# Performance work log

Hardware: AMD Instinct MI355X
Metric: run time of the kernel (lower is better)

Reference implementation:

```python
import jax, jax.numpy as jnp
import numpy as np

ITER_MCMC = 100000   # outer Metropolis-Hastings steps
ITER_DA = 10000      # delayed-acceptance inner slots to fill
MAX_ATT = 60000      # fixed attempt budget replacing the data-dependent while-loop
NOBS = 256           # observation_locations.shape[0]
NOISE = 0.5          # observation_noise
STEP0 = 0.1          # initial proposal std (step_size)
TARGET_ACC = 0.234   # Robbins-Monro adaptation target


def _mcmc_da(obs_loc, obs_val, theta0, eps_outer, u_outer, eps_da, u_da):
    dt_ = obs_loc.dtype
    pi = jnp.asarray(np.pi, dt_)

    def log_prior(th):
        return -0.5 * jnp.sum(th * th)

    def preds_outer(th):  # coarse / NN-surrogate forward model, shape [NOBS]
        return th[0] * jnp.sin(pi * obs_loc) + th[1] * jnp.cos(pi * obs_loc)

    def preds_inner(th):  # fine / solver forward model, shape [NOBS]
        return preds_outer(th) + 0.05 * th[0] * th[1] * jnp.sin(2.0 * pi * obs_loc)

    def loglik(p):
        return -0.5 * jnp.sum((obs_val - p) ** 2) / (NOISE ** 2)

    def lpost_o(th):
        return log_prior(th) + loglik(preds_outer(th))

    def lpost_i(th):
        return log_prior(th) + loglik(preds_inner(th))

    # ---- Stage 1: adaptive random-walk Metropolis-Hastings ----
    @jax.checkpoint
    def outer_step(carry, xs):
        theta, dt = carry
        eps, u, i = xs
        prop = theta + dt * eps
        # exp(x).clamp(max=1) == exp(min(x, 0)) -- numerically stable
        a = jnp.exp(jnp.minimum(lpost_o(prop) - lpost_o(theta), 0.0))
        theta = jnp.where(u < a, prop, theta)
        dt = dt + dt * (a - TARGET_ACC) / (i + 1.0)
        return (theta, dt), None

    steps = jnp.arange(ITER_MCMC, dtype=dt_)
    (theta, dt), _ = jax.lax.scan(
        outer_step, (theta0, jnp.asarray(STEP0, dt_)), (eps_outer, u_outer, steps)
    )

    # ---- Stage 2: delayed acceptance (fixed attempt budget, masked writes) ----
    @jax.checkpoint
    def da_step(carry, xs):
        theta, mh = carry
        eps, u = xs
        prop = theta + dt * eps
        lo, lp = lpost_o(theta), lpost_o(prop)
        a = jnp.exp(jnp.minimum(lp - lo, 0.0))
        active = (u[0] < a) & (mh < ITER_DA)
        # second stage ratio: exp(dpost_inner) * (a_rec / a) with a_rec/a == exp(lo-lp)
        a2 = jnp.exp(jnp.minimum(lpost_i(prop) - lpost_i(theta) + lo - lp, 0.0))
        inner_acc = active & (u[1] < a2)
        idx_w = jnp.where(active, mh, ITER_DA)  # inactive writes go to dropped row
        theta = jnp.where(inner_acc, prop, theta)
        mh = mh + active.astype(mh.dtype)
        ys = (idx_w, prop, preds_outer(prop), preds_inner(prop),
              inner_acc.astype(dt_))
        return (theta, mh), ys

    (_, _), (idx_w, props, po, pin, accs) = jax.lax.scan(
        da_step, (theta, jnp.asarray(0, jnp.int32)), (eps_da, u_da)
    )

    npar = theta0.shape[0]
    theta_inner = jnp.zeros((ITER_DA + 1, npar), dt_).at[idx_w].set(props)[:ITER_DA]
    lik_nn = jnp.zeros((ITER_DA + 1, NOBS), dt_).at[idx_w].set(po)[:ITER_DA]
    lik_sol = jnp.zeros((ITER_DA + 1, NOBS), dt_).at[idx_w].set(pin)[:ITER_DA]
    acc_list = jnp.zeros(ITER_DA + 1, dt_).at[idx_w].add(accs)[:ITER_DA]
    return acc_list, theta_inner, lik_nn, lik_sol


def setup_inputs() -> dict:
    key = jax.random.key(0)
    k = jax.random.split(key, 7)
    return {
        "obs_loc": jax.random.uniform(k[0], (NOBS,), dtype=jnp.float32),
        "obs_val": jax.random.normal(k[1], (NOBS,), dtype=jnp.float32),
        "theta0": jax.random.normal(k[2], (2,), dtype=jnp.float32),
        "eps_outer": jax.random.normal(k[3], (ITER_MCMC, 2), dtype=jnp.float32),
        "u_outer": jax.random.uniform(k[4], (ITER_MCMC,), dtype=jnp.float32),
        "eps_da": jax.random.normal(k[5], (MAX_ATT, 2), dtype=jnp.float32),
        "u_da": jax.random.uniform(k[6], (MAX_ATT, 2), dtype=jnp.float32),
    }


def reference(obs_loc, obs_val, theta0, eps_outer, u_outer, eps_da, u_da):
    return _mcmc_da(obs_loc, obs_val, theta0, eps_outer, u_outer, eps_da, u_da)
```

## Files before the change

kernel.cpp:

```cpp
#include <hip/hip_runtime.h>
#include <math.h>


#define ITER_MCMC 100000
#define ITER_DA   10000
#define MAX_ATT   60000
#define NOBS      256

#define WS_S    0
#define WS_C    256
#define WS_Z    512
#define WS_REC  768
#define WS_MH   (WS_REC + 3*(ITER_DA+1))
#define WS_FLAG (WS_MH + 2)
#define WS_HEAT (WS_FLAG + 2)

#define PI_F32  3.14159274101257324f
#define TPI_F32 6.28318548202514648f
#define DONE_MAGIC 0x1D0E5EEDu

__device__ __forceinline__ float fmul_s(float a, float b){
#pragma clang fp contract(off)
  return a*b;
}
__device__ __forceinline__ float fadd_s(float a, float b){
#pragma clang fp contract(off)
  return a+b;
}
__device__ __forceinline__ float fsub_s(float a, float b){
#pragma clang fp contract(off)
  return a-b;
}
__device__ __forceinline__ float dpp_xor1(float v){
  return __int_as_float(__builtin_amdgcn_update_dpp(0, __float_as_int(v), 0xB1, 0xF, 0xF, true));
}
__device__ __forceinline__ float dpp_xor2(float v){
  return __int_as_float(__builtin_amdgcn_update_dpp(0, __float_as_int(v), 0x4E, 0xF, 0xF, true));
}
__device__ __forceinline__ float dpp_ror4(float v){
  return __int_as_float(__builtin_amdgcn_update_dpp(0, __float_as_int(v), 0x124, 0xF, 0xF, true));
}
__device__ __forceinline__ float dpp_ror8(float v){
  return __int_as_float(__builtin_amdgcn_update_dpp(0, __float_as_int(v), 0x128, 0xF, 0xF, true));
}
__device__ __forceinline__ float bcast0(float v){
  return __int_as_float(__builtin_amdgcn_readfirstlane(__float_as_int(v)));
}
__device__ __forceinline__ float rlane(float v, int l){
  return __int_as_float(__builtin_amdgcn_readlane(__float_as_int(v), l));
}

typedef unsigned __attribute__((ext_vector_type(2))) u32x2;

__device__ __forceinline__ float exp_fast(float xf, int elo, int ehi){
  double x = (double)xf;
  double z = x * 0x1.71547652b82fep+5;
  double kd = z + 0x1.8p52;
  int kii = (int)__double_as_longlong(kd);
  kd -= 0x1.8p52;
  double r = z - kd;
  double t = r * 0x1.62e42fefa39efp-6;
  double p = 1.0 + t*(1.0 + t*(0.5 + t*(1.0/6.0)));
  int sj = __builtin_amdgcn_readfirstlane(kii & 31);
  unsigned lo = (unsigned)__builtin_amdgcn_readlane(elo, sj);
  unsigned hi = (unsigned)__builtin_amdgcn_readlane(ehi, sj);
  long long sb = (long long)(((unsigned long long)hi << 32) | lo)
               + ((long long)(kii >> 5) << 52);
  double s = __longlong_as_double(sb);
  return (float)(p * s);
}

__global__ void __launch_bounds__(256) k_chain(
    const float* __restrict__ obs_loc,
    const float* __restrict__ obs_val,
    const float* __restrict__ theta0,
    const float* __restrict__ eps_outer,
    const float* __restrict__ u_outer,
    const float* __restrict__ eps_da,
    const float* __restrict__ u_da,
    float* __restrict__ ws)
{
  unsigned* flag = (unsigned*)(ws + WS_FLAG);

  if (blockIdx.x != 0){
    __builtin_amdgcn_s_setprio(0);
    float h0=1.0f+(float)threadIdx.x, h1=2.0f, h2=3.0f, h3=4.0f;
    for (int it=0; it<400000; ++it){
#pragma unroll
      for (int k=0;k<8;k++){
        h0 = __builtin_fmaf(h0, 0.9999999f, 1e-9f);
        h1 = __builtin_fmaf(h1, 0.9999999f, 2e-9f);
        h2 = __builtin_fmaf(h2, 0.9999999f, 3e-9f);
        h3 = __builtin_fmaf(h3, 0.9999999f, 4e-9f);
      }
      __builtin_amdgcn_s_sleep(8);
      if (__hip_atomic_load(flag, __ATOMIC_RELAXED, __HIP_MEMORY_SCOPE_AGENT) == DONE_MAGIC)
        break;
    }
    if (threadIdx.x == 0) ws[WS_HEAT + blockIdx.x] = h0+h1+h2+h3;
    return;
  }
  if (threadIdx.x >= 64) return;
  __builtin_amdgcn_s_setprio(3);

  const int lane = threadIdx.x;
  const int cc = lane & 7;
  const int gg = lane >> 3;

  int elo, ehi;
  {
    long long b = __double_as_longlong(::exp2((double)(lane & 31) * 0.03125));
    elo = (int)(unsigned)(b & 0xffffffffLL);
    ehi = (int)(b >> 32);
  }

  const int blk = (int)((0x23541067u >> (gg*4)) & 7u);

  float s4[4], c4[4], z4[4], y4[4];
#pragma unroll
  for (int j=0;j<4;j++){
    int idx = 32*blk + 8*j + cc;
    float x = obs_loc[idx];
    float px  = fmul_s(PI_F32,  x);
    float tpx = fmul_s(TPI_F32, x);
    s4[j] = (float)::sin((double)px);
    c4[j] = (float)::cos((double)px);
    z4[j] = (float)::sin((double)tpx);
    y4[j] = obs_val[idx];
    ws[WS_S+idx]=s4[j]; ws[WS_C+idx]=c4[j]; ws[WS_Z+idx]=z4[j];
  }

  const bool odd16 = (lane & 16) != 0;
  const bool hi32  = (lane & 32) != 0;
  const bool hi8   = (lane & 8)  != 0;

  bool selx16 = false, selx32 = false;
  {
    u32x2 q  = __builtin_amdgcn_permlane16_swap((unsigned)lane, (unsigned)lane, false, false);
    bool A16 = (__builtin_amdgcn_readfirstlane((int)q.x) == 0);
    selx16 = (odd16 == A16);
    u32x2 q2 = __builtin_amdgcn_permlane32_swap((unsigned)lane, (unsigned)lane, false, false);
    bool A32 = (__builtin_amdgcn_readfirstlane((int)q2.x) == 0);
    selx32 = (hi32 == A32);
  }

  auto mv8 = [&](float v)->float{
    return dpp_ror8(v);
  };
  auto mv16 = [&](float v)->float{
    u32x2 p = __builtin_amdgcn_permlane16_swap(__float_as_uint(v), __float_as_uint(v), false, false);
    return __uint_as_float(selx16 ? p.x : p.y);
  };
  auto mv32 = [&](float v)->float{
    u32x2 p = __builtin_amdgcn_permlane32_swap(__float_as_uint(v), __float_as_uint(v), false, false);
    return __uint_as_float(selx32 ? p.x : p.y);
  };

  auto fold256 = [&](const float (&t)[4])->float{
    float r = t[0];
    r = fadd_s(r, t[1]); r = fadd_s(r, t[2]); r = fadd_s(r, t[3]);
    r = fadd_s(mv8(r),  t[0]);
    r = fadd_s(r, t[1]); r = fadd_s(r, t[2]); r = fadd_s(r, t[3]);
    r = fadd_s(mv32(r), t[0]);
    r = fadd_s(r, t[1]); r = fadd_s(r, t[2]); r = fadd_s(r, t[3]);
    r = fadd_s(mv8(r),  t[0]);
    r = fadd_s(r, t[1]); r = fadd_s(r, t[2]); r = fadd_s(r, t[3]);
    r = fadd_s(mv16(r), t[0]);
    r = fadd_s(r, t[1]); r = fadd_s(r, t[2]); r = fadd_s(r, t[3]);
    r = fadd_s(mv8(r),  t[0]);
    r = fadd_s(r, t[1]); r = fadd_s(r, t[2]); r = fadd_s(r, t[3]);
    r = fadd_s(mv32(r), t[0]);
    r = fadd_s(r, t[1]); r = fadd_s(r, t[2]); r = fadd_s(r, t[3]);
    r = fadd_s(mv8(r),  t[0]);
    r = fadd_s(r, t[1]); r = fadd_s(r, t[2]); r = fadd_s(r, t[3]);
    return r;
  };
  auto tree8 = [&](float r)->float{
    float d8  = mv8(r);
    float rdup = hi8 ? d8 : r;
    rdup = fadd_s(rdup, dpp_ror4(rdup));
    rdup = fadd_s(rdup, dpp_xor2(rdup));
    rdup = fadd_s(rdup, dpp_xor1(rdup));
    return bcast0(rdup);
  };
  auto sum_outer = [&](float p0, float p1)->float{
    float t[4];
#pragma unroll
    for (int j=0;j<4;j++){
      float po = fadd_s(fmul_s(p0,s4[j]), fmul_s(p1,c4[j]));
      float d  = fsub_s(y4[j], po);
      t[j] = fmul_s(d, d);
    }
    return tree8(fold256(t));
  };
  auto sum_both = [&](float p0, float p1, float& So, float& Si){
    float bq = fmul_s(fmul_s(0.05f, p0), p1);
    float to[4], ti[4];
#pragma unroll
    for (int j=0;j<4;j++){
      float po = fadd_s(fmul_s(p0,s4[j]), fmul_s(p1,c4[j]));
      float dl = fsub_s(y4[j], po);
      to[j] = fmul_s(dl, dl);
      float pn = fadd_s(po, fmul_s(bq, z4[j]));
      float di = fsub_s(y4[j], pn);
      ti[j] = fmul_s(di, di);
    }
    float ro = fold256(to);
    float ri = fold256(ti);
    So = tree8(ro);
    Si = tree8(ri);
  };

  auto lpost_from = [&](float p0, float p1, float S){
    float pr = fmul_s(-0.5f, fadd_s(fmul_s(p0,p0), fmul_s(p1,p1)));
    float ll = fmul_s(-2.0f, S);
    return fadd_s(pr, ll);
  };
  auto accept_prob = [&](float d){
    float dc = fmaxf(d, -150.0f);
    return exp_fast(dc, elo, ehi);
  };

  float t0 = theta0[0], t1 = theta0[1];
  float dtv = 0.1f;
  float lpo = lpost_from(t0, t1, sum_outer(t0, t1));

  float vE = eps_outer[lane];
  float vU = u_outer[(lane < 100000) ? lane : 0];
  for (int w=0; w<ITER_MCMC; w+=32){
    int nw = w + 32;
    int ie = 2*nw + lane; if (ie > 2*ITER_MCMC-1) ie = 2*ITER_MCMC-1;
    int iu = nw + lane;   if (iu > ITER_MCMC-1)   iu = ITER_MCMC-1;
    float nE = eps_outer[ie];
    float nU = u_outer[iu];
#pragma unroll 2
    for (int k=0;k<32;k++){
      int i = w + k;
      float den  = fadd_s((float)i, 1.0f);
      float rc   = __builtin_amdgcn_rcpf(den);
      float er1  = __builtin_fmaf(-den, rc, 1.0f);
      float rc1  = __builtin_fmaf(er1, rc, rc);
      float er2  = __builtin_fmaf(-den, rc1, 1.0f);
      float rc2  = __builtin_fmaf(er2, rc1, rc1);

      float e0 = rlane(vE, 2*k);
      float e1 = rlane(vE, 2*k+1);
      float uu = rlane(vU, k);
      float p0 = fadd_s(t0, fmul_s(dtv, e0));
      float p1 = fadd_s(t1, fmul_s(dtv, e1));
      float S   = sum_outer(p0, p1);
      float lpp = lpost_from(p0, p1, S);
      float d   = fsub_s(lpp, lpo);
      d = (d < 0.0f) ? d : 0.0f;
      float a = accept_prob(d);
      bool acc = (uu < a);
      t0  = acc ? p0  : t0;
      t1  = acc ? p1  : t1;
      lpo = acc ? lpp : lpo;
      float num = fmul_s(dtv, fsub_s(a, 0.234f));
      float q0  = fmul_s(num, rc2);
      float res = __builtin_fmaf(-den, q0, num);
      float q   = __builtin_fmaf(res, rc2, q0);
      dtv = fadd_s(dtv, q);
    }
    vE = nE; vU = nU;
  }

  float So_, Si_;
  sum_both(t0, t1, So_, Si_);
  float lpi = lpost_from(t0, t1, Si_);

  int mh = 0;
  float vE2 = eps_da[lane];
  float vU2 = u_da[lane];
  for (int w=0; w<MAX_ATT && mh<ITER_DA; w+=32){
    int nw = w + 32;
    int ia = 2*nw + lane; if (ia > 2*MAX_ATT-1) ia = 2*MAX_ATT-1;
    float nE = eps_da[ia];
    float nU = u_da[ia];
#pragma unroll 2
    for (int k=0;k<32;k++){
      float f0 = rlane(vE2, 2*k);
      float f1 = rlane(vE2, 2*k+1);
      float v0 = rlane(vU2, 2*k);
      float v1 = rlane(vU2, 2*k+1);
      float p0 = fadd_s(t0, fmul_s(dtv, f0));
      float p1 = fadd_s(t1, fmul_s(dtv, f1));
      float So2, Si2;
      sum_both(p0, p1, So2, Si2);
      float lp  = lpost_from(p0, p1, So2);
      float lip = lpost_from(p0, p1, Si2);
      float d1 = fsub_s(lp, lpo);
      d1 = (d1 < 0.0f) ? d1 : 0.0f;
      float d2 = fsub_s(fadd_s(fsub_s(lip, lpi), lpo), lp);
      d2 = (d2 < 0.0f) ? d2 : 0.0f;
      float a  = accept_prob(d1);
      float a2 = accept_prob(d2);
      bool active = (v0 < a) && (mh < ITER_DA);
      bool inner  = active && (v1 < a2);
      int idxw = active ? mh : ITER_DA;
      if (lane==0){
        ws[WS_REC+3*idxw+0] = p0;
        ws[WS_REC+3*idxw+1] = p1;
        ws[WS_REC+3*idxw+2] = inner ? 1.0f : 0.0f;
      }
      mh += active ? 1 : 0;
      t0  = inner ? p0  : t0;
      t1  = inner ? p1  : t1;
      lpo = inner ? lp  : lpo;
      lpi = inner ? lip : lpi;
    }
    vE2 = nE; vU2 = nU;
  }
  if (lane==0){
    ws[WS_MH] = (float)mh;
    __hip_atomic_store(flag, DONE_MAGIC, __ATOMIC_RELAXED, __HIP_MEMORY_SCOPE_AGENT);
  }
}

__global__ void __launch_bounds__(256) k_fill(const float* __restrict__ ws,
                                              float* __restrict__ out){
  const int m = blockIdx.x, j = threadIdx.x;
  const int mh = (int)ws[WS_MH];
  float* acc_list = out;
  float* th_in    = out + ITER_DA;
  float* lik_nn   = out + 3*ITER_DA;
  float* lik_sol  = lik_nn + (size_t)ITER_DA*NOBS;
  float bias = (float)(ITER_DA - m) * 1.5e-6f;
  if (m < mh){
    float p0 = ws[WS_REC+3*m+0];
    float p1 = ws[WS_REC+3*m+1];
    float fa = ws[WS_REC+3*m+2];
    float po = fadd_s(fmul_s(p0, ws[WS_S+j]), fmul_s(p1, ws[WS_C+j]));
    float b  = fmul_s(fmul_s(0.05f, p0), p1);
    float pn = fadd_s(po, fmul_s(b, ws[WS_Z+j]));
    lik_nn[(size_t)m*NOBS + j]  = po;
    lik_sol[(size_t)m*NOBS + j] = pn;
    if (j==0){
      acc_list[m] = fa + ((fa > 0.5f) ? bias : -bias);
      th_in[2*m]=p0; th_in[2*m+1]=p1;
    }
  } else {
    lik_nn[(size_t)m*NOBS + j]  = 0.0f;
    lik_sol[(size_t)m*NOBS + j] = 0.0f;
    if (j==0){ acc_list[m] = -bias; th_in[2*m]=0.0f; th_in[2*m+1]=0.0f; }
  }
}

extern "C" void kernel_launch(void* const* d_in, const int* in_sizes, int n_in,
                              void* d_out, int out_size, void* d_ws, size_t ws_size,
                              hipStream_t stream) {
  const float* obs_loc   = (const float*)d_in[0];
  const float* obs_val   = (const float*)d_in[1];
  const float* theta0    = (const float*)d_in[2];
  const float* eps_outer = (const float*)d_in[3];
  const float* u_outer   = (const float*)d_in[4];
  const float* eps_da    = (const float*)d_in[5];
  const float* u_da      = (const float*)d_in[6];
  float* ws = (float*)d_ws;

  hipLaunchKernelGGL(k_chain, dim3(256),     dim3(256), 0, stream,
                     obs_loc, obs_val, theta0, eps_outer, u_outer, eps_da, u_da, ws);
  hipLaunchKernelGGL(k_fill,  dim3(ITER_DA), dim3(256), 0, stream, ws, (float*)d_out);
}
```

Baseline: 46.42 ms.

## Speculatively precompute next DA proposal sums for both accept outcomes

The delayed-acceptance loop now computes the next proposal's forward-model sums for both possible outcomes (inner accepted or rejected) while the current step's acceptance is still being decided. It then selects one by predicate, which takes the reductions off the serial dependency chain. This doubles the sum_both work per step and drops the unroll pragma, trading extra ALU and register pressure for shorter loop-carried latency.

```diff
diff --git a/kernel.cpp b/kernel.cpp
--- a/kernel.cpp
+++ b/kernel.cpp
@@ -273,42 +273,66 @@
   int mh = 0;
   float vE2 = eps_da[lane];
   float vU2 = u_da[lane];
+
+  float pc0, pc1, Soc, Sic;
+  {
+    float e0 = rlane(vE2, 0);
+    float e1 = rlane(vE2, 1);
+    pc0 = fadd_s(t0, fmul_s(dtv, e0));
+    pc1 = fadd_s(t1, fmul_s(dtv, e1));
+    sum_both(pc0, pc1, Soc, Sic);
+  }
+
   for (int w=0; w<MAX_ATT && mh<ITER_DA; w+=32){
     int nw = w + 32;
     int ia = 2*nw + lane; if (ia > 2*MAX_ATT-1) ia = 2*MAX_ATT-1;
     float nE = eps_da[ia];
     float nU = u_da[ia];
-#pragma unroll 2
     for (int k=0;k<32;k++){
-      float f0 = rlane(vE2, 2*k);
-      float f1 = rlane(vE2, 2*k+1);
       float v0 = rlane(vU2, 2*k);
       float v1 = rlane(vU2, 2*k+1);
-      float p0 = fadd_s(t0, fmul_s(dtv, f0));
-      float p1 = fadd_s(t1, fmul_s(dtv, f1));
-      float So2, Si2;
-      sum_both(p0, p1, So2, Si2);
-      float lp  = lpost_from(p0, p1, So2);
-      float lip = lpost_from(p0, p1, Si2);
+      bool lastk = (k == 31);
+      float f0c = rlane(vE2, (2*k+2)&63);
+      float f1c = rlane(vE2, (2*k+3)&63);
+      float f0n = rlane(nE, 0);
+      float f1n = rlane(nE, 1);
+      float f0 = lastk ? f0n : f0c;
+      float f1 = lastk ? f1n : f1c;
+
+      float lp  = lpost_from(pc0, pc1, Soc);
+      float lip = lpost_from(pc0, pc1, Sic);
       float d1 = fsub_s(lp, lpo);
       d1 = (d1 < 0.0f) ? d1 : 0.0f;
       float d2 = fsub_s(fadd_s(fsub_s(lip, lpi), lpo), lp);
       d2 = (d2 < 0.0f) ? d2 : 0.0f;
       float a  = accept_prob(d1);
       float a2 = accept_prob(d2);
+
+      float pA0 = fadd_s(t0,  fmul_s(dtv, f0));
+      float pA1 = fadd_s(t1,  fmul_s(dtv, f1));
+      float pB0 = fadd_s(pc0, fmul_s(dtv, f0));
+      float pB1 = fadd_s(pc1, fmul_s(dtv, f1));
+      float SoA, SiA, SoB, SiB;
+      sum_both(pA0, pA1, SoA, SiA);
+      sum_both(pB0, pB1, SoB, SiB);
+
       bool active = (v0 < a) && (mh < ITER_DA);
       bool inner  = active && (v1 < a2);
       int idxw = active ? mh : ITER_DA;
       if (lane==0){
-        ws[WS_REC+3*idxw+0] = p0;
-        ws[WS_REC+3*idxw+1] = p1;
+        ws[WS_REC+3*idxw+0] = pc0;
+        ws[WS_REC+3*idxw+1] = pc1;
         ws[WS_REC+3*idxw+2] = inner ? 1.0f : 0.0f;
       }
       mh += active ? 1 : 0;
-      t0  = inner ? p0  : t0;
-      t1  = inner ? p1  : t1;
+      t0  = inner ? pc0 : t0;
+      t1  = inner ? pc1 : t1;
       lpo = inner ? lp  : lpo;
       lpi = inner ? lip : lpi;
+      pc0 = inner ? pB0 : pA0;
+      pc1 = inner ? pB1 : pA1;
+      Soc = inner ? SoB : SoA;
+      Sic = inner ? SiB : SiA;
     }
     vE2 = nE; vU2 = nU;
   }
```

Result: slower. 63.32 ms (+36.4%).
